# Kernel optimization log

Measured on AMD Instinct MI355X. Metric: run time of the kernel, lower is better.

The kernel has to match this reference:

```python
import jax, jax.numpy as jnp
import numpy as np

CH, K, RR = 12, 7, 4  # pooled temporal size / involution kernel / reduction ratio

def conv3d(x, w, pad):
    return jax.lax.conv_general_dilated(x, w, (1, 1, 1), [(pad, pad)] * 3,
                                        dimension_numbers=('NCDHW', 'OIDHW', 'NCDHW'))

def conv1x1(x, w, b=None):
    out = jnp.einsum('oi,bidhw->bodhw', w, x)
    return out if b is None else out + b[None, :, None, None, None]

def adaptive_pool(x, outs):
    b, c, D, H, W = x.shape
    fd, fh, fw = D // outs[0], H // outs[1], W // outs[2]
    return x.reshape(b, c, outs[0], fd, outs[1], fh, outs[2], fw).mean(axis=(3, 5, 7))

def bnorm(x, g, b):
    m = x.mean(axis=(0, 2, 3, 4), keepdims=True)
    v = x.var(axis=(0, 2, 3, 4), keepdims=True)
    return (x - m) * jax.lax.rsqrt(v + 1e-5) * g[None, :, None, None, None] + b[None, :, None, None, None]

def setup_inputs():
    key = jax.random.key(0)
    ks = jax.random.split(key, 12)
    c = 64; cr = c // RR; Cf = c + CH * cr; M = CH * K * K
    def nrm(k_, shape, fan_in):
        return jax.random.normal(k_, shape, jnp.float32) / np.sqrt(fan_in)
    return {
        'x_CT': jax.random.normal(ks[0], (2, c, 8, 56, 56), jnp.float32),
        'x_WSI': jax.random.normal(ks[1], (2, c, 12, 56, 56), jnp.float32),
        'W_ct': nrm(ks[2], (c, c), c), 'b_ct': jnp.zeros((c,), jnp.float32),
        'W_wsi': nrm(ks[3], (c, c), c), 'b_wsi': jnp.zeros((c,), jnp.float32),
        'W_att': nrm(ks[4], (1 + CH, M, 5, 5, 5), M * 125),
        'W_inv': nrm(ks[5], (K * K, M), M), 'b_inv': jnp.zeros((K * K,), jnp.float32),
        'W_rr': nrm(ks[6], (cr, c, 3, 3, 3), c * 27),
        'g1': jnp.ones((Cf,), jnp.float32), 'be1': jnp.zeros((Cf,), jnp.float32),
        'g2': jnp.ones((Cf,), jnp.float32), 'be2': jnp.zeros((Cf,), jnp.float32),
        'W_p1': nrm(ks[7], (Cf, Cf), Cf), 'b_p1': jnp.zeros((Cf,), jnp.float32),
        'W_p2': nrm(ks[8], (c, Cf), Cf), 'b_p2': jnp.zeros((c,), jnp.float32),
    }

def reference(x_CT, x_WSI, W_ct, b_ct, W_wsi, b_wsi, W_att, W_inv, b_inv, W_rr,
              g1, be1, g2, be2, W_p1, b_p1, W_p2, b_p2):
    b, c, t, h, w = x_CT.shape
    cr = c // RR
    M = CH * K * K
    x1 = conv1x1(x_CT, W_ct, b_ct)
    xw1 = adaptive_pool(conv1x1(x_WSI, W_wsi, b_wsi), (CH, K, K))       # (b,c,CH,K,K)
    # cross-modal bmm: (b, thw, c) x (b, c, M) -> (b, thw, M)
    multi = jnp.einsum('bnc,bcm->bnm', x1.reshape(b, c, t * h * w).transpose(0, 2, 1),
                       xw1.reshape(b, c, M))
    feature = multi.reshape(b, t, h, w, M).transpose(0, 4, 1, 2, 3)     # (b,M,t,h,w)
    Att = jax.nn.sigmoid(conv3d(feature, W_att, 2))                      # (b,1+CH,t,h,w)
    xw3 = conv3d(x_WSI, W_rr, 1)                                         # (b,cr,CH,h,w)
    xw5 = jnp.broadcast_to(xw3.reshape(b, cr * CH, 1, h, w), (b, cr * CH, t, h, w))
    x_FS = jnp.concatenate([x_CT, xw5], axis=1)                          # (b,Cf,t,h,w)
    Att_CT = jnp.broadcast_to(Att[:, :1], (b, c, t, h, w))
    Att_WSI = jnp.tile(Att[:, 1:].reshape(b, CH, t, h * w), (1, 1, cr, 1)).reshape(b, CH * cr, t, h, w)
    Att_FS = jnp.concatenate([Att_CT, Att_WSI], axis=1)
    x_Att = x_FS * Att_FS + x_FS
    # per-pixel dynamic kernel: (b,t,K,K,h,w)
    kern = conv1x1(feature, W_inv, b_inv).transpose(0, 2, 1, 3, 4).reshape(b, t, K, K, h, w)
    x_Att1 = jax.nn.relu(bnorm(conv1x1(x_Att, W_p1, b_p1), g1, be1))
    pad = K // 2
    xp = jnp.pad(x_Att1, ((0, 0), (0, 0), (0, 0), (pad, pad), (pad, pad)))
    out = jnp.zeros_like(x_Att1)
    for i in range(K):                                                   # fixed 7x7 involution taps
        for j in range(K):
            out = out + kern[:, None, :, i, j] * xp[:, :, :, i:i + h, j:j + w]
    return conv1x1(bnorm(out, g2, be2) + x_Att, W_p2, b_p2)
```

## Files before the change

### kernel.cpp

```cpp
#include <hip/hip_runtime.h>
#include <hip/hip_bf16.h>
#include <math.h>

typedef __hip_bfloat16 bf16;
typedef unsigned short us;
typedef __attribute__((ext_vector_type(8))) short short8v;
typedef __attribute__((ext_vector_type(4))) float f32x4;
#define DEV static __device__ __forceinline__
DEV float b2f(bf16 x){ return __bfloat162float(x); }
DEV bf16  f2b(float x){ return __float2bfloat16(x); }
DEV us    f2u(float x){ bf16 h=f2b(x); return *(us*)&h; }
DEV float u2f(us u){ return __uint_as_float(((unsigned)u)<<16); }
DEV float blo(unsigned int w){ return __uint_as_float(w<<16); }
DEV float bhi(unsigned int w){ return __uint_as_float(w&0xffff0000u); }
DEV float ldin(const void* p, long i, int f){
  return f ? ((const float*)p)[i] : b2f(((const bf16*)p)[i]);
}

#define PP 25088

#define X1o    0L
#define POOLo  3211264L
#define XW1o   3286528L
#define WXo    3361792L
#define WXTo   3569792L
#define WIXo   3825792L
#define ATTo   3832064L
#define KERNo  4484352L
#define XW3o   6942976L
#define STATo  8147200L
#define FLAGo  8149248L
#define WFo    8149264L
#define WATTFo 8267280L
#define WINVFo 9222784L
#define BF16o  9251600L
#define X1To   KERNo
#define WRR2o  WXo
#define bXCT   0L
#define bXWSI  3211264L
#define bXATT  8028160L
#define bY1    20873216L
#define bINV   20873216L
#define bXATT1 33718272L
#define bWP1B  46563328L
#define bWP2B  46628864L
#define bW2S   46645248L
#define bXWT   bY1
#define oWCT   0
#define oBCT   4096
#define oWWSI  4160
#define oBWSI  8256
#define oWRR   8320
#define oBINV  35968
#define oWP1   36032
#define oWP2   101568
#define oBP2   117952

__global__ void k_detect(const us* raw, int* flag){
  int t = threadIdx.x;
  us u = raw[2*t];
  int e = (u>>7)&0xFF;
  int hit = (e >= 137);
  unsigned long long m = __ballot(hit);
  if(t==0) flag[0] = (__popcll(m) >= 8) ? 1 : 0;
}

__global__ void k_c2b(const void* src, bf16* dst, int n, const int* flag){
  int i = blockIdx.x*256+threadIdx.x; if(i>=n) return;
  int f = flag[0];
  dst[i] = f ? f2b(((const float*)src)[i]) : ((const bf16*)src)[i];
}
__global__ void k_c2f(const void* src, float* dst, int n, const int* flag){
  int i = blockIdx.x*256+threadIdx.x; if(i>=n) return;
  dst[i] = ldin(src, i, flag[0]);
}

__global__ void k_cvt(const void* Wct,const void* bct,const void* Wwsi,const void* bwsi,
                      const void* Wrr,const void* binv,const void* Wp1,const void* Wp2,
                      const void* bp2,float* wf,const int* flag){
  int i = blockIdx.x*256 + threadIdx.x;
  int f = flag[0];
  if (i < 4096){ int co=i>>6, ci=i&63; wf[oWCT + ci*64+co] = ldin(Wct,i,f); }
  else if (i < 4160){ wf[i] = ldin(bct,i-4096,f); }
  else if (i < 8256){ wf[i] = ldin(Wwsi,i-4160,f); }
  else if (i < 8320){ wf[i] = ldin(bwsi,i-8256,f); }
  else if (i < 35968){ int l=i-8320; int co=l/1728, r=l%1728, ci=r/27, tp=r%27;
                       wf[oWRR + (ci*27+tp)*16+co] = ldin(Wrr,l,f); }
  else if (i < 36017){ wf[oBINV + (i-35968)] = ldin(binv,i-35968,f); }
  else if (i < 36032){ }
  else if (i < 101568){ int l=i-36032; int co=l>>8, ci=l&255; wf[oWP1 + ci*256+co] = ldin(Wp1,l,f); }
  else if (i < 117952){ int l=i-101568; int o=l>>8, ci=l&255; wf[oWP2 + ci*64+o] = ldin(Wp2,l,f); }
  else if (i < 118016){ int l=i-117952; if(l<64) wf[oBP2 + l] = ldin(bp2,l,f); }
}

__global__ void k_wb(const void* Wp1, const void* Wp2, us* Wp1b, us* Wp2b, const int* flag){
  int i = blockIdx.x*256+threadIdx.x;
  int f = flag[0];
  if(i<65536) Wp1b[i]=f2u(ldin(Wp1,i,f));
  else if(i<81920) Wp2b[i-65536]=f2u(ldin(Wp2,i-65536,f));
}

__global__ void k_pool(const bf16* xwsi, float* pool){
  int i = blockIdx.x*256+threadIdx.x;
  int c = i&63; int m=(i>>6)%588; int b=i/37632;
  int d=m/49, r=m%49, ii=r/7, jj=r%7;
  const bf16* src = xwsi + ((size_t)(b*64+c)*12 + d)*3136 + (ii*8)*56 + jj*8;
  float s=0;
  for(int u=0;u<8;u++) for(int v=0;v<8;v++) s += b2f(src[u*56+v]);
  pool[i] = s*(1.f/64.f);
}

__global__ void k_wsit(const bf16* xwsib, us* xwt){
  __shared__ us tl[64*68];
  int tid=threadIdx.x; int p0=blockIdx.x*64; int d=blockIdx.y; int b=blockIdx.z;
  #pragma unroll
  for(int k=0;k<16;k++){
    int idx=k*256+tid; int px=idx&63, c=idx>>6;
    bf16 h = xwsib[((size_t)(b*64+c)*12+d)*3136 + p0+px];
    tl[px*68+c] = *(us*)&h;
  }
  __syncthreads();
  #pragma unroll
  for(int k=0;k<16;k++){
    int idx=k*256+tid; int px=idx>>6, ch=idx&63;
    xwt[((size_t)(b*12+d)*3136 + p0+px)*64 + ch] = tl[px*68+ch];
  }
}

__global__ void k_xw1(const float* pool, const float* wf, float* xw1){
  int i = blockIdx.x*256+threadIdx.x;
  int c = i&63; int m=(i>>6)%588; int b=i/37632;
  const float* p = pool + (b*588+m)*64;
  const float* w = wf + oWWSI + c*64;
  float s = wf[oBWSI + c];
  for(int ci=0;ci<64;ci++) s += w[ci]*p[ci];
  xw1[i]=s;
}

__global__ void k_Wx(const float* Wattf, const float* xw1, float* Wx){
  int i = blockIdx.x*256+threadIdx.x; if(i>=208000) return;
  int c=i&63; int r=i>>6; int tap=r%125; int o=(r/125)%13; int b=r/1625;
  const float* wa = Wattf + (size_t)o*588*125 + tap;
  const float* xp = xw1 + b*588*64 + c;
  float s=0;
  for(int m=0;m<588;m++) s += wa[(size_t)m*125] * xp[m*64];
  Wx[i]=s;
}

__global__ void k_Wfrag(const float* Wx, us* Wf){
  int i = blockIdx.x*256+threadIdx.x; if(i>=256000) return;
  int j=i&7; int m=(i>>3)&15; int kg=(i>>7)&3; int ch=(i>>9)&1;
  int r=i>>10; int tap=r%125; int b=r/125;
  int c = ch*32 + kg*8 + j;
  float v = (m<13) ? Wx[((size_t)(b*13+m)*125+tap)*64 + c] : 0.f;
  Wf[i] = f2u(v);
}

__global__ void k_rrfrag(const float* wf, us* Wrr2){
  int i = blockIdx.x*256+threadIdx.x; if(i>=27648) return;
  int j=i&7; int l=(i>>3)&63; int kg=(i>>9)&1; int td=i>>10;
  int m=l&15, g=l>>4;
  int c = kg*32 + g*8 + j;
  Wrr2[i] = f2u(wf[oWRR + (c*27+td)*16 + m]);
}

__global__ void k_Winvx(const float* Winvf, const float* xw1, float* Wix){
  int i = blockIdx.x*256+threadIdx.x; if(i>=6272) return;
  int kk=i%49; int c=(i/49)&63; int b=i/3136;
  const float* xp = xw1 + b*588*64 + c;
  float s=0;
  for(int m=0;m<588;m++) s += Winvf[kk*588+m] * xp[m*64];
  Wix[i]=s;
}

__global__ void k_x1(const bf16* xct, const float* wf, float* x1, us* x1t){
  int p = blockIdx.x*256+threadIdx.x;
  int co0 = blockIdx.y*16; int b = blockIdx.z;
  float acc[16];
  #pragma unroll
  for(int o=0;o<16;o++) acc[o]=wf[oBCT+co0+o];
  const bf16* xp = xct + (size_t)b*64*PP + p;
  for(int ci=0;ci<64;ci++){
    float xv = b2f(xp[(size_t)ci*PP]);
    const float* w = wf + oWCT + ci*64 + co0;
    #pragma unroll
    for(int o=0;o<16;o++) acc[o] += w[o]*xv;
  }
  float* out = x1 + ((size_t)b*64+co0)*PP + p;
  #pragma unroll
  for(int o=0;o<16;o++) out[(size_t)o*PP]=acc[o];
  unsigned int pk[8];
  #pragma unroll
  for(int o2=0;o2<8;o2++)
    pk[o2] = (unsigned)f2u(acc[2*o2]) | ((unsigned)f2u(acc[2*o2+1])<<16);
  us* xo = x1t + ((size_t)(b*PP)+p)*64 + co0;
  *(uint4*)xo     = make_uint4(pk[0],pk[1],pk[2],pk[3]);
  *(uint4*)(xo+8) = make_uint4(pk[4],pk[5],pk[6],pk[7]);
}

__global__ __launch_bounds__(256) void k_att(const us* x1t, const us* Wf, float* att){
  __shared__ short xt[10368];
  int tid=threadIdx.x;
  int tile=blockIdx.x, t=blockIdx.y, b=blockIdx.z;
  int y0=(tile/7)*8, x0=(tile%7)*8;
  int w=tid>>6, l=tid&63;
  int pc=l&7, pr=(l>>3)&1, g=l>>4;
  f32x4 acc0={0,0,0,0}, acc1={0,0,0,0};
  int bbase = ((2*w+pr)*12 + pc)*72 + g*8;
  const us* Wb = Wf + (size_t)b*128000 + l*8;
  for(int dt=0;dt<5;dt++){
    int ti=t+dt-2;
    if(ti<0||ti>=8) continue;
    __syncthreads();
    for(int e=tid;e<1152;e+=256){
      int px=e>>3, q=e&7;
      int row=px/12, col=px-row*12;
      int gy=y0+row-2, gx=x0+col-2;
      uint4 v={0,0,0,0};
      if((unsigned)gy<56u && (unsigned)gx<56u)
        v = *(const uint4*)(x1t + ((size_t)(b*PP) + ti*3136 + gy*56 + gx)*64 + q*8);
      *(uint4*)&xt[px*72 + q*8] = v;
    }
    __syncthreads();
    const us* Wd = Wb + dt*25600;
    #pragma unroll
    for(int dy=0;dy<5;dy++){
      #pragma unroll
      for(int dx=0;dx<5;dx++){
        int off = bbase + dy*864 + dx*72;
        short8v a0 = *(const short8v*)(Wd + (dy*5+dx)*1024);
        short8v b0 = *(const short8v*)&xt[off];
        acc0 = __builtin_amdgcn_mfma_f32_16x16x32_bf16(a0,b0,acc0,0,0,0);
        short8v a1 = *(const short8v*)(Wd + (dy*5+dx)*1024 + 512);
        short8v b1 = *(const short8v*)&xt[off+32];
        acc1 = __builtin_amdgcn_mfma_f32_16x16x32_bf16(a1,b1,acc1,0,0,0);
      }
    }
  }
  int px=l&15; int epc=px&7, epr=px>>3;
  size_t pbase=(size_t)t*3136+(size_t)(y0+2*w+epr)*56+x0+epc;
  #pragma unroll
  for(int r=0;r<4;r++){
    int o=g*4+r;
    if(o<13){
      float s=acc0[r]+acc1[r];
      att[((size_t)b*13+o)*PP+pbase]=1.f/(1.f+__expf(-s));
    }
  }
}

__global__ void k_kern(const float* x1, const float* Wix, const float* wf, float* kern){
  int p = blockIdx.x*256+threadIdx.x; int b=blockIdx.y;
  float acc[49];
  #pragma unroll
  for(int kk=0;kk<49;kk++) acc[kk]=wf[oBINV+kk];
  const float* xp = x1 + (size_t)b*64*PP + p;
  for(int c=0;c<64;c++){
    float xv = xp[(size_t)c*PP];
    const float* w = Wix + (b*64+c)*49;
    #pragma unroll
    for(int kk=0;kk<49;kk++) acc[kk]+=w[kk]*xv;
  }
  float* out = kern + (size_t)b*49*PP + p;
  #pragma unroll
  for(int kk=0;kk<49;kk++) out[(size_t)kk*PP]=acc[kk];
}

__global__ __launch_bounds__(256) void k_rr(const us* xwt, const us* Wrr2, bf16* xw3){
  __shared__ short xt[7200];
  int tid=threadIdx.x;
  int tile=blockIdx.x, d=blockIdx.y, b=blockIdx.z;
  int y0=(tile/7)*8, x0=(tile%7)*8;
  int w=tid>>6, l=tid&63;
  int pc=l&7, pr=(l>>3)&1, g=l>>4;
  f32x4 acc0={0,0,0,0}, acc1={0,0,0,0};
  int bbase = ((2*w+pr)*10 + pc)*72 + g*8;
  const us* Wl = Wrr2 + l*8;
  for(int dz=0;dz<3;dz++){
    int di=d+dz-1;
    if(di<0||di>=12) continue;
    __syncthreads();
    for(int e=tid;e<800;e+=256){
      int px=e>>3, q=e&7;
      int row=px/10, col=px-row*10;
      int gy=y0+row-1, gx=x0+col-1;
      uint4 v={0,0,0,0};
      if((unsigned)gy<56u && (unsigned)gx<56u)
        v = *(const uint4*)(xwt + ((size_t)(b*12+di)*3136 + gy*56 + gx)*64 + q*8);
      *(uint4*)&xt[px*72 + q*8] = v;
    }
    __syncthreads();
    const us* Wd = Wl + dz*9216;
    #pragma unroll
    for(int tap=0;tap<9;tap++){
      int dy=tap/3, dx=tap-dy*3;
      int off = bbase + (dy*10+dx)*72;
      short8v a0 = *(const short8v*)(Wd + tap*1024);
      short8v b0 = *(const short8v*)&xt[off];
      acc0 = __builtin_amdgcn_mfma_f32_16x16x32_bf16(a0,b0,acc0,0,0,0);
      short8v a1 = *(const short8v*)(Wd + tap*1024 + 512);
      short8v b1 = *(const short8v*)&xt[off+32];
      acc1 = __builtin_amdgcn_mfma_f32_16x16x32_bf16(a1,b1,acc1,0,0,0);
    }
  }
  int px=l&15; int epc=px&7, epr=px>>3;
  size_t pp=(size_t)(y0+2*w+epr)*56 + x0+epc;
  #pragma unroll
  for(int r=0;r<4;r++){
    int o=g*4+r;
    xw3[((size_t)(b*16+o)*12+d)*3136 + pp] = f2b(acc0[r]+acc1[r]);
  }
}

__global__ void k_xatt(const bf16* xct, const bf16* xw3, const float* att, us* xattT){
  __shared__ us tl[64*258];
  int tid=threadIdx.x; int p0=blockIdx.x*64; int b=blockIdx.y;
  for(int k=0;k<64;k++){
    int idx=k*256+tid; int ch=idx>>6, pp=idx&63;
    int p=p0+pp;
    float v;
    if(ch<64){
      v = b2f(xct[((size_t)b*64+ch)*PP+p]) * (1.f+att[(size_t)b*13*PP+p]);
    } else {
      int q=ch-64; int co=q/12, dd=q-co*12;
      int s=p%3136;
      v = b2f(xw3[((size_t)(b*16+co)*12+dd)*3136+s]) * (1.f+att[((size_t)b*13+1+q/16)*PP+p]);
    }
    tl[pp*258+ch]=f2u(v);
  }
  __syncthreads();
  for(int k=0;k<64;k++)
    xattT[((size_t)b*PP + p0+k)*256 + tid] = tl[k*258+tid];
}

__global__ __launch_bounds__(256) void k_p1(const us* xattT, const us* Wp1b, us* y1T){
  __shared__ us wt[16384];
  int tid=threadIdx.x; int w=tid>>6, l=tid&63;
  int pt=blockIdx.x, qtr=blockIdx.y, b=blockIdx.z;
  int co0 = qtr*64;
  #pragma unroll
  for(int it=0;it<8;it++){
    int f = it*256+tid;
    int n=f>>9, kc=(f>>6)&7, lane=f&63;
    int co = co0 + n*16 + (lane&15);
    int ci = (lane>>4)*8 + kc*32;
    uint4 v = *(const uint4*)(Wp1b + (size_t)co*256 + ci);
    *(uint4*)(wt + f*8) = v;
  }
  __syncthreads();
  int p0 = pt*64 + w*16;
  const us* xa = xattT + ((size_t)b*PP + p0 + (l&15))*256 + ((l>>4)*8);
  f32x4 acc[4];
  #pragma unroll
  for(int n=0;n<4;n++) acc[n]=(f32x4){0,0,0,0};
  for(int kc=0;kc<8;kc++){
    short8v a = *(const short8v*)(xa + kc*32);
    #pragma unroll
    for(int n=0;n<4;n++){
      short8v bf = *(const short8v*)(wt + ((n*8+kc)*64 + l)*8);
      acc[n] = __builtin_amdgcn_mfma_f32_16x16x32_bf16(a,bf,acc[n],0,0,0);
    }
  }
  int col=l&15, rowb=(l>>4)*4;
  us* yo = y1T + ((size_t)b*PP + p0)*256 + co0;
  #pragma unroll
  for(int n=0;n<4;n++)
    #pragma unroll
    for(int r=0;r<4;r++)
      yo[(size_t)(rowb+r)*256 + n*16 + col] = f2u(acc[n][r]);
}

__global__ void k_stats(const us* src, float* sum, float* sq){
  int tid=threadIdx.x; int pt=blockIdx.x, b=blockIdx.y;
  const us* p = src + ((size_t)b*PP + pt*64)*256 + tid;
  float s=0,q=0;
  #pragma unroll 8
  for(int i=0;i<64;i++){ float v=u2f(p[(size_t)i*256]); s+=v; q+=v*v; }
  atomicAdd(&sum[tid],s); atomicAdd(&sq[tid],q);
}
__global__ void k_finstat(const float* sum, const float* sq, const void* g, const void* be,
                          const int* flag, float* sc, float* sh){
  int ch=threadIdx.x;
  int f=flag[0];
  float m = sum[ch]*(1.f/50176.f);
  float v = sq[ch]*(1.f/50176.f) - m*m;
  float s = ldin(g,ch,f) * rsqrtf(v+1e-5f);
  sc[ch]=s; sh[ch]=ldin(be,ch,f) - m*s;
}

__global__ void k_bn1(const us* y1T, const float* sc, const float* sh, us* xatt1){
  size_t i = ((size_t)blockIdx.x*256+threadIdx.x)*8;
  int ch0 = (int)(i & 255);
  uint4 v = *(const uint4*)(y1T+i);
  const us* up=(const us*)&v;
  us r[8];
  #pragma unroll
  for(int j=0;j<8;j++){
    float x = u2f(up[j]);
    x = x*sc[ch0+j]+sh[ch0+j]; x = x>0.f?x:0.f;
    r[j]=f2u(x);
  }
  *(uint4*)(xatt1+i) = *(const uint4*)r;
}

__global__ __launch_bounds__(256) void k_inv(const bf16* xatt1, const float* kern, us* invT){
  __shared__ __align__(16) us xt[196*72];
  int tid=threadIdx.x;
  int bx=blockIdx.x, by=blockIdx.y, bz=blockIdx.z;
  int t=bz&7, b=bz>>3;
  int y0=(bx/7)*8, x0=(bx%7)*8, c0=by*64;
  int w=tid>>6, l=tid&63;
  int ty=l>>3, tx=l&7;
  for(int e=tid;e<1568;e+=256){
    int row=e>>3, seg=e&7;
    int yy=row/14, xx=row%14;
    int gy=y0+yy-3, gx=x0+xx-3;
    uint4 v={0,0,0,0};
    if(gy>=0&&gy<56&&gx>=0&&gx<56)
      v = *(const uint4*)&xatt1[((size_t)b*PP + t*3136 + gy*56+gx)*256 + c0 + seg*8];
    *(uint4*)&xt[row*72+seg*8]=v;
  }
  float kr[49];
  size_t pxs=(size_t)t*3136 + (y0+ty)*56 + x0+tx;
  #pragma unroll
  for(int kk=0;kk<49;kk++) kr[kk]=kern[((size_t)b*49+kk)*PP+pxs];
  __syncthreads();
  #pragma unroll
  for(int s=0;s<2;s++){
    int sub=2*w+s;
    float acc[8];
    #pragma unroll
    for(int e=0;e<8;e++) acc[e]=0;
    for(int i=0;i<7;i++){
      #pragma unroll
      for(int j=0;j<7;j++){
        uint4 u = *(const uint4*)&xt[((ty+i)*14+tx+j)*72 + sub*8];
        float kv = kr[i*7+j];
        acc[0]+=kv*blo(u.x); acc[1]+=kv*bhi(u.x);
        acc[2]+=kv*blo(u.y); acc[3]+=kv*bhi(u.y);
        acc[4]+=kv*blo(u.z); acc[5]+=kv*bhi(u.z);
        acc[6]+=kv*blo(u.w); acc[7]+=kv*bhi(u.w);
      }
    }
    unsigned pk[4];
    #pragma unroll
    for(int e=0;e<4;e++)
      pk[e] = (unsigned)f2u(acc[2*e]) | ((unsigned)f2u(acc[2*e+1])<<16);
    *(uint4*)&invT[((size_t)b*PP+pxs)*256 + c0 + sub*8] = make_uint4(pk[0],pk[1],pk[2],pk[3]);
  }
}

__global__ void k_w2s(const float* wf, const float* sc2, const float* sh2,
                      us* W2sb, float* bias2){
  __shared__ float red[256];
  int o=blockIdx.x, ci=threadIdx.x;
  float wv = wf[oWP2 + ci*64 + o];
  W2sb[o*256+ci] = f2u(wv * sc2[ci]);
  red[ci] = wv * sh2[ci];
  __syncthreads();
  for(int st=128;st>0;st>>=1){ if(ci<st) red[ci]+=red[ci+st]; __syncthreads(); }
  if(ci==0) bias2[o] = wf[oBP2+o] + red[0];
}

__global__ __launch_bounds__(256) void k_final(const us* invT, const us* xattT,
                                               const us* W2sb, const us* Wp2b,
                                               const float* bias2, float* out){
  __shared__ us wt[32768];
  int tid=threadIdx.x; int w=tid>>6, l=tid&63;
  int pt=blockIdx.x, b=blockIdx.y;
  #pragma unroll
  for(int it=0;it<16;it++){
    int f = it*256+tid;
    int which = f>>11;
    int g = f&2047;
    int n=g>>9, kc=(g>>6)&7, lane=g&63;
    int co = n*16 + (lane&15);
    int ci = (lane>>4)*8 + kc*32;
    const us* src = which ? Wp2b : W2sb;
    uint4 v = *(const uint4*)(src + (size_t)co*256 + ci);
    *(uint4*)(wt + f*8) = v;
  }
  __syncthreads();
  int p0 = pt*64 + w*16;
  size_t abase = ((size_t)b*PP + p0 + (l&15))*256 + ((l>>4)*8);
  f32x4 acc[4];
  #pragma unroll
  for(int n=0;n<4;n++) acc[n]=(f32x4){0,0,0,0};
  for(int kc=0;kc<8;kc++){
    short8v ai = *(const short8v*)(invT + abase + kc*32);
    short8v ax = *(const short8v*)(xattT + abase + kc*32);
    #pragma unroll
    for(int n=0;n<4;n++){
      short8v b1 = *(const short8v*)(wt + ((n*8+kc)*64 + l)*8);
      acc[n] = __builtin_amdgcn_mfma_f32_16x16x32_bf16(ai,b1,acc[n],0,0,0);
      short8v b2 = *(const short8v*)(wt + 16384 + ((n*8+kc)*64 + l)*8);
      acc[n] = __builtin_amdgcn_mfma_f32_16x16x32_bf16(ax,b2,acc[n],0,0,0);
    }
  }
  int col=l&15, rowb=(l>>4)*4;
  #pragma unroll
  for(int n=0;n<4;n++){
    float bb = bias2[n*16+col];
    #pragma unroll
    for(int r=0;r<4;r++)
      out[((size_t)b*64 + n*16+col)*PP + p0 + rowb + r] = acc[n][r] + bb;
  }
}

extern "C" void kernel_launch(void* const* d_in, const int* in_sizes, int n_in,
                              void* d_out, int out_size, void* d_ws, size_t ws_size,
                              hipStream_t stream){
  const void* xct_r =d_in[0];
  const void* xwsi_r=d_in[1];
  const void* Wct =d_in[2];
  const void* bct =d_in[3];
  const void* Wwsi=d_in[4];
  const void* bwsi=d_in[5];
  const void* Watt=d_in[6];
  const void* Winv=d_in[7];
  const void* binv=d_in[8];
  const void* Wrr =d_in[9];
  const void* g1  =d_in[10];
  const void* be1 =d_in[11];
  const void* g2  =d_in[12];
  const void* be2 =d_in[13];
  const void* Wp1 =d_in[14];
  const void* Wp2 =d_in[16];
  const void* bp2 =d_in[17];
  float* ws=(float*)d_ws;
  float* x1=ws+X1o; float* pool=ws+POOLo; float* xw1=ws+XW1o;
  float* Wx=ws+WXo; float* Wix=ws+WIXo;
  float* att=ws+ATTo; float* kern=ws+KERNo;
  us* Wf=(us*)(ws+WXTo);
  us* Wrr2=(us*)(ws+WRR2o);
  us* x1t=(us*)(ws+X1To);
  bf16* xw3=(bf16*)(ws+XW3o);
  float* stat=ws+STATo; float* wf=ws+WFo;
  float* Wattf=ws+WATTFo; float* Winvf=ws+WINVFo;
  float* bias2=ws+WATTFo;
  int* flag=(int*)(ws+FLAGo);
  bf16* bfb=(bf16*)(ws+BF16o);
  bf16* xctb=bfb+bXCT; bf16* xwsib=bfb+bXWSI;
  us* xattT=(us*)(bfb+bXATT); us* y1T=(us*)(bfb+bY1); us* invT=(us*)(bfb+bINV);
  bf16* xatt1=bfb+bXATT1;
  us* Wp1b=(us*)(bfb+bWP1B); us* Wp2b=(us*)(bfb+bWP2B); us* W2sb=(us*)(bfb+bW2S);
  us* xwt=(us*)(bfb+bXWT);
  float* sum1=stat; float* sq1=stat+256; float* sum2=stat+512; float* sq2=stat+768;
  float* sc1=stat+1024; float* sh1=stat+1280; float* sc2=stat+1536; float* sh2=stat+1792;

  hipMemsetAsync(stat,0,4096,stream);
  k_detect<<<1,64,0,stream>>>((const us*)xct_r,flag);
  k_c2b   <<<12544,256,0,stream>>>(xct_r,xctb,3211264,flag);
  k_c2b   <<<18816,256,0,stream>>>(xwsi_r,xwsib,4816896,flag);
  k_c2f   <<<3733,256,0,stream>>>(Watt,Wattf,955500,flag);
  k_c2f   <<<113,256,0,stream>>>(Winv,Winvf,28812,flag);
  k_cvt   <<<461,256,0,stream>>>(Wct,bct,Wwsi,bwsi,Wrr,binv,Wp1,Wp2,bp2,wf,flag);
  k_wb    <<<320,256,0,stream>>>(Wp1,Wp2,Wp1b,Wp2b,flag);
  k_wsit  <<<dim3(49,12,2),256,0,stream>>>(xwsib,xwt);
  k_pool  <<<294,256,0,stream>>>(xwsib,pool);
  k_xw1   <<<294,256,0,stream>>>(pool,wf,xw1);
  k_Wx    <<<813,256,0,stream>>>(Wattf,xw1,Wx);
  k_Wfrag <<<1000,256,0,stream>>>(Wx,Wf);
  k_rrfrag<<<108,256,0,stream>>>(wf,Wrr2);
  k_Winvx <<<25,256,0,stream>>>(Winvf,xw1,Wix);
  k_x1    <<<dim3(98,4,2),256,0,stream>>>(xctb,wf,x1,x1t);
  k_att   <<<dim3(49,8,2),256,0,stream>>>(x1t,Wf,att);
  k_kern  <<<dim3(98,2),256,0,stream>>>(x1,Wix,wf,kern);
  k_rr    <<<dim3(49,12,2),256,0,stream>>>(xwt,Wrr2,xw3);
  k_xatt  <<<dim3(392,2),256,0,stream>>>(xctb,xw3,att,xattT);
  k_p1    <<<dim3(392,4,2),256,0,stream>>>(xattT,Wp1b,y1T);
  k_stats <<<dim3(392,2),256,0,stream>>>(y1T,sum1,sq1);
  k_finstat<<<1,256,0,stream>>>(sum1,sq1,g1,be1,flag,sc1,sh1);
  k_bn1   <<<6272,256,0,stream>>>(y1T,sc1,sh1,(us*)xatt1);
  k_inv   <<<dim3(49,4,16),256,0,stream>>>(xatt1,kern,invT);
  k_stats <<<dim3(392,2),256,0,stream>>>(invT,sum2,sq2);
  k_finstat<<<1,256,0,stream>>>(sum2,sq2,g2,be2,flag,sc2,sh2);
  k_w2s   <<<64,256,0,stream>>>(wf,sc2,sh2,W2sb,bias2);
  k_final <<<dim3(392,2),256,0,stream>>>(invT,xattT,W2sb,Wp2b,bias2,(float*)d_out);
}
```

Baseline: 395.4 us.

## Fuse input conversion, BN1 apply and x1 storage into consumer kernels

Several passes over intermediates are removed. The WSI bf16 conversion pass is dropped: the transpose kernel now reads the raw input directly, and pooling reads the transposed buffer. The fp32 x1 output is removed, so the dynamic-kernel generator reads the channel-last bf16 x1t with vector loads. The BN1 scale/shift plus ReLU kernel is folded into the involution tile load, which also drops the xatt1 buffer. Together these cut memory traffic and launches. In exchange, pooling reads strided along the channel-last layout, and kern is now computed from bf16 rather than fp32 x1, which reduces precision.

```diff
diff --git a/kernel.cpp b/kernel.cpp
--- a/kernel.cpp
+++ b/kernel.cpp
@@ -34,14 +34,12 @@
 #define WATTFo 8267280L
 #define WINVFo 9222784L
 #define BF16o  9251600L
-#define X1To   KERNo
 #define WRR2o  WXo
 #define bXCT   0L
-#define bXWSI  3211264L
+#define bX1T   3211264L
 #define bXATT  8028160L
 #define bY1    20873216L
-#define bINV   20873216L
-#define bXATT1 33718272L
+#define bINV   33718272L
 #define bWP1B  46563328L
 #define bWP2B  46628864L
 #define bW2S   46645248L
@@ -100,31 +98,33 @@
   else if(i<81920) Wp2b[i-65536]=f2u(ldin(Wp2,i-65536,f));
 }
 
-__global__ void k_pool(const bf16* xwsi, float* pool){
+__global__ void k_wsit(const void* xwsi_r, const int* flag, us* xwt){
+  __shared__ us tl[64*68];
+  int tid=threadIdx.x; int p0=blockIdx.x*64; int d=blockIdx.y; int b=blockIdx.z;
+  int f=flag[0];
+  #pragma unroll
+  for(int k=0;k<16;k++){
+    int idx=k*256+tid; int px=idx&63, c=idx>>6;
+    float v = ldin(xwsi_r, ((long)(b*64+c)*12+d)*3136 + p0+px, f);
+    tl[px*68+c] = f2u(v);
+  }
+  __syncthreads();
+  #pragma unroll
+  for(int k=0;k<16;k++){
+    int idx=k*256+tid; int px=idx>>6, ch=idx&63;
+    xwt[((size_t)(b*12+d)*3136 + p0+px)*64 + ch] = tl[px*68+ch];
+  }
+}
+
+__global__ void k_pool(const us* xwt, float* pool){
   int i = blockIdx.x*256+threadIdx.x;
   int c = i&63; int m=(i>>6)%588; int b=i/37632;
   int d=m/49, r=m%49, ii=r/7, jj=r%7;
-  const bf16* src = xwsi + ((size_t)(b*64+c)*12 + d)*3136 + (ii*8)*56 + jj*8;
+  const us* src = xwt + ((size_t)(b*12+d)*3136 + (ii*8)*56 + jj*8)*64 + c;
   float s=0;
-  for(int u=0;u<8;u++) for(int v=0;v<8;v++) s += b2f(src[u*56+v]);
+  for(int u=0;u<8;u++)
+    for(int v=0;v<8;v++) s += u2f(src[(size_t)(u*56+v)*64]);
   pool[i] = s*(1.f/64.f);
-}
-
-__global__ void k_wsit(const bf16* xwsib, us* xwt){
-  __shared__ us tl[64*68];
-  int tid=threadIdx.x; int p0=blockIdx.x*64; int d=blockIdx.y; int b=blockIdx.z;
-  #pragma unroll
-  for(int k=0;k<16;k++){
-    int idx=k*256+tid; int px=idx&63, c=idx>>6;
-    bf16 h = xwsib[((size_t)(b*64+c)*12+d)*3136 + p0+px];
-    tl[px*68+c] = *(us*)&h;
-  }
-  __syncthreads();
-  #pragma unroll
-  for(int k=0;k<16;k++){
-    int idx=k*256+tid; int px=idx>>6, ch=idx&63;
-    xwt[((size_t)(b*12+d)*3136 + p0+px)*64 + ch] = tl[px*68+ch];
-  }
 }
 
 __global__ void k_xw1(const float* pool, const float* wf, float* xw1){
@@ -173,7 +173,7 @@
   Wix[i]=s;
 }
 
-__global__ void k_x1(const bf16* xct, const float* wf, float* x1, us* x1t){
+__global__ void k_x1(const bf16* xct, const float* wf, us* x1t){
   int p = blockIdx.x*256+threadIdx.x;
   int co0 = blockIdx.y*16; int b = blockIdx.z;
   float acc[16];
@@ -186,9 +186,6 @@
     #pragma unroll
     for(int o=0;o<16;o++) acc[o] += w[o]*xv;
   }
-  float* out = x1 + ((size_t)b*64+co0)*PP + p;
-  #pragma unroll
-  for(int o=0;o<16;o++) out[(size_t)o*PP]=acc[o];
   unsigned int pk[8];
   #pragma unroll
   for(int o2=0;o2<8;o2++)
@@ -249,17 +246,23 @@
   }
 }
 
-__global__ void k_kern(const float* x1, const float* Wix, const float* wf, float* kern){
+__global__ void k_kern(const us* x1t, const float* Wix, const float* wf, float* kern){
   int p = blockIdx.x*256+threadIdx.x; int b=blockIdx.y;
   float acc[49];
   #pragma unroll
   for(int kk=0;kk<49;kk++) acc[kk]=wf[oBINV+kk];
-  const float* xp = x1 + (size_t)b*64*PP + p;
-  for(int c=0;c<64;c++){
-    float xv = xp[(size_t)c*PP];
-    const float* w = Wix + (b*64+c)*49;
-    #pragma unroll
-    for(int kk=0;kk<49;kk++) acc[kk]+=w[kk]*xv;
+  const us* xp = x1t + ((size_t)b*PP + p)*64;
+  #pragma unroll
+  for(int c8=0;c8<8;c8++){
+    uint4 v = *(const uint4*)(xp + c8*8);
+    const us* vp=(const us*)&v;
+    #pragma unroll
+    for(int j=0;j<8;j++){
+      float xv = u2f(vp[j]);
+      const float* w = Wix + (b*64+c8*8+j)*49;
+      #pragma unroll
+      for(int kk=0;kk<49;kk++) acc[kk]+=w[kk]*xv;
+    }
   }
   float* out = kern + (size_t)b*49*PP + p;
   #pragma unroll
@@ -388,22 +391,8 @@
   sc[ch]=s; sh[ch]=ldin(be,ch,f) - m*s;
 }
 
-__global__ void k_bn1(const us* y1T, const float* sc, const float* sh, us* xatt1){
-  size_t i = ((size_t)blockIdx.x*256+threadIdx.x)*8;
-  int ch0 = (int)(i & 255);
-  uint4 v = *(const uint4*)(y1T+i);
-  const us* up=(const us*)&v;
-  us r[8];
-  #pragma unroll
-  for(int j=0;j<8;j++){
-    float x = u2f(up[j]);
-    x = x*sc[ch0+j]+sh[ch0+j]; x = x>0.f?x:0.f;
-    r[j]=f2u(x);
-  }
-  *(uint4*)(xatt1+i) = *(const uint4*)r;
-}
-
-__global__ __launch_bounds__(256) void k_inv(const bf16* xatt1, const float* kern, us* invT){
+__global__ __launch_bounds__(256) void k_inv(const us* y1T, const float* sc1, const float* sh1,
+                                             const float* kern, us* invT){
   __shared__ __align__(16) us xt[196*72];
   int tid=threadIdx.x;
   int bx=blockIdx.x, by=blockIdx.y, bz=blockIdx.z;
@@ -411,14 +400,28 @@
   int y0=(bx/7)*8, x0=(bx%7)*8, c0=by*64;
   int w=tid>>6, l=tid&63;
   int ty=l>>3, tx=l&7;
+  int segb = c0 + (tid&7)*8;
+  float scr[8], shr[8];
+  #pragma unroll
+  for(int j=0;j<8;j++){ scr[j]=sc1[segb+j]; shr[j]=sh1[segb+j]; }
   for(int e=tid;e<1568;e+=256){
     int row=e>>3, seg=e&7;
     int yy=row/14, xx=row%14;
     int gy=y0+yy-3, gx=x0+xx-3;
-    uint4 v={0,0,0,0};
-    if(gy>=0&&gy<56&&gx>=0&&gx<56)
-      v = *(const uint4*)&xatt1[((size_t)b*PP + t*3136 + gy*56+gx)*256 + c0 + seg*8];
-    *(uint4*)&xt[row*72+seg*8]=v;
+    uint4 o4={0,0,0,0};
+    if(gy>=0&&gy<56&&gx>=0&&gx<56){
+      uint4 v = *(const uint4*)&y1T[((size_t)b*PP + t*3136 + gy*56+gx)*256 + c0 + seg*8];
+      const us* vp=(const us*)&v;
+      us r[8];
+      #pragma unroll
+      for(int j=0;j<8;j++){
+        float x = u2f(vp[j]);
+        x = x*scr[j]+shr[j]; x = x>0.f?x:0.f;
+        r[j]=f2u(x);
+      }
+      o4 = *(const uint4*)r;
+    }
+    *(uint4*)&xt[row*72+seg*8]=o4;
   }
   float kr[49];
   size_t pxs=(size_t)t*3136 + (y0+ty)*56 + x0+tx;
@@ -528,21 +531,20 @@
   const void* Wp2 =d_in[16];
   const void* bp2 =d_in[17];
   float* ws=(float*)d_ws;
-  float* x1=ws+X1o; float* pool=ws+POOLo; float* xw1=ws+XW1o;
+  float* pool=ws+POOLo; float* xw1=ws+XW1o;
   float* Wx=ws+WXo; float* Wix=ws+WIXo;
   float* att=ws+ATTo; float* kern=ws+KERNo;
   us* Wf=(us*)(ws+WXTo);
   us* Wrr2=(us*)(ws+WRR2o);
-  us* x1t=(us*)(ws+X1To);
   bf16* xw3=(bf16*)(ws+XW3o);
   float* stat=ws+STATo; float* wf=ws+WFo;
   float* Wattf=ws+WATTFo; float* Winvf=ws+WINVFo;
   float* bias2=ws+WATTFo;
   int* flag=(int*)(ws+FLAGo);
   bf16* bfb=(bf16*)(ws+BF16o);
-  bf16* xctb=bfb+bXCT; bf16* xwsib=bfb+bXWSI;
+  bf16* xctb=bfb+bXCT;
+  us* x1t=(us*)(bfb+bX1T);
   us* xattT=(us*)(bfb+bXATT); us* y1T=(us*)(bfb+bY1); us* invT=(us*)(bfb+bINV);
-  bf16* xatt1=bfb+bXATT1;
   us* Wp1b=(us*)(bfb+bWP1B); us* Wp2b=(us*)(bfb+bWP2B); us* W2sb=(us*)(bfb+bW2S);
   us* xwt=(us*)(bfb+bXWT);
   float* sum1=stat; float* sq1=stat+256; float* sum2=stat+512; float* sq2=stat+768;
@@ -551,28 +553,26 @@
   hipMemsetAsync(stat,0,4096,stream);
   k_detect<<<1,64,0,stream>>>((const us*)xct_r,flag);
   k_c2b   <<<12544,256,0,stream>>>(xct_r,xctb,3211264,flag);
-  k_c2b   <<<18816,256,0,stream>>>(xwsi_r,xwsib,4816896,flag);
   k_c2f   <<<3733,256,0,stream>>>(Watt,Wattf,955500,flag);
   k_c2f   <<<113,256,0,stream>>>(Winv,Winvf,28812,flag);
   k_cvt   <<<461,256,0,stream>>>(Wct,bct,Wwsi,bwsi,Wrr,binv,Wp1,Wp2,bp2,wf,flag);
   k_wb    <<<320,256,0,stream>>>(Wp1,Wp2,Wp1b,Wp2b,flag);
-  k_wsit  <<<dim3(49,12,2),256,0,stream>>>(xwsib,xwt);
-  k_pool  <<<294,256,0,stream>>>(xwsib,pool);
+  k_wsit  <<<dim3(49,12,2),256,0,stream>>>(xwsi_r,flag,xwt);
+  k_pool  <<<294,256,0,stream>>>(xwt,pool);
   k_xw1   <<<294,256,0,stream>>>(pool,wf,xw1);
   k_Wx    <<<813,256,0,stream>>>(Wattf,xw1,Wx);
   k_Wfrag <<<1000,256,0,stream>>>(Wx,Wf);
   k_rrfrag<<<108,256,0,stream>>>(wf,Wrr2);
   k_Winvx <<<25,256,0,stream>>>(Winvf,xw1,Wix);
-  k_x1    <<<dim3(98,4,2),256,0,stream>>>(xctb,wf,x1,x1t);
+  k_x1    <<<dim3(98,4,2),256,0,stream>>>(xctb,wf,x1t);
   k_att   <<<dim3(49,8,2),256,0,stream>>>(x1t,Wf,att);
-  k_kern  <<<dim3(98,2),256,0,stream>>>(x1,Wix,wf,kern);
+  k_kern  <<<dim3(98,2),256,0,stream>>>(x1t,Wix,wf,kern);
   k_rr    <<<dim3(49,12,2),256,0,stream>>>(xwt,Wrr2,xw3);
   k_xatt  <<<dim3(392,2),256,0,stream>>>(xctb,xw3,att,xattT);
   k_p1    <<<dim3(392,4,2),256,0,stream>>>(xattT,Wp1b,y1T);
   k_stats <<<dim3(392,2),256,0,stream>>>(y1T,sum1,sq1);
   k_finstat<<<1,256,0,stream>>>(sum1,sq1,g1,be1,flag,sc1,sh1);
-  k_bn1   <<<6272,256,0,stream>>>(y1T,sc1,sh1,(us*)xatt1);
-  k_inv   <<<dim3(49,4,16),256,0,stream>>>(xatt1,kern,invT);
+  k_inv   <<<dim3(49,4,16),256,0,stream>>>(y1T,sc1,sh1,kern,invT);
   k_stats <<<dim3(392,2),256,0,stream>>>(invT,sum2,sq2);
   k_finstat<<<1,256,0,stream>>>(sum2,sq2,g2,be2,flag,sc2,sh2);
   k_w2s   <<<64,256,0,stream>>>(wf,sc2,sh2,W2sb,bias2);
```

Measured after the change: 387.5 us. 2.0% less time.
